# Kernel tuning notes

Measured on AMD Instinct MI355X. Metric: run time of the kernel, lower is better.

## Reference

```python
import jax, jax.numpy as jnp
import numpy as np

N_USER, N_MOVIE, N_EDGE = 200_000, 100_000, 4_000_000
D = 64  # feature dim = hidden_channels


def setup_inputs() -> dict:
    key = jax.random.key(0)
    ks = jax.random.split(key, 18)

    def W(k):
        return (jax.random.normal(k, (D, D), jnp.float32) / np.sqrt(D)).astype(jnp.float32)

    inp = {
        "x_user": jax.random.normal(ks[0], (N_USER, D), jnp.float32),
        "x_movie": jax.random.normal(ks[1], (N_MOVIE, D), jnp.float32),
        # layer 1, relation user->movie and movie->user
        "Wl1_um": W(ks[2]), "Wr1_um": W(ks[3]), "b1_um": jnp.zeros((D,), jnp.float32),
        "Wl1_mu": W(ks[4]), "Wr1_mu": W(ks[5]), "b1_mu": jnp.zeros((D,), jnp.float32),
        # layer 2
        "Wl2_um": W(ks[6]), "Wr2_um": W(ks[7]), "b2_um": jnp.zeros((D,), jnp.float32),
        "Wl2_mu": W(ks[8]), "Wr2_mu": W(ks[9]), "b2_mu": jnp.zeros((D,), jnp.float32),
        # rating edges: user_idx[e] rates movie_idx[e]; reverse relation reuses them swapped
        "user_idx": jax.random.randint(ks[10], (N_EDGE,), 0, N_USER, jnp.int64 if jax.config.jax_enable_x64 else jnp.int32),
        "movie_idx": jax.random.randint(ks[11], (N_EDGE,), 0, N_MOVIE, jnp.int64 if jax.config.jax_enable_x64 else jnp.int32),
    }
    return inp


def _sage(x_src, x_dst, src_idx, dst_idx, Wl, bl, Wr, n_dst):
    # PyG SAGEConv: lin_l(mean_aggr(x_j)) + bias + lin_r(x_dst)
    msg = x_src[src_idx]                                   # [E, D] gather
    s = jax.ops.segment_sum(msg, dst_idx, num_segments=n_dst)
    cnt = jax.ops.segment_sum(jnp.ones((msg.shape[0], 1), msg.dtype), dst_idx,
                              num_segments=n_dst)
    mean = s / jnp.maximum(cnt, 1.0)                       # degree-0 rows -> 0
    return mean @ Wl + bl + x_dst @ Wr


def reference(x_user, x_movie,
              Wl1_um, Wr1_um, b1_um, Wl1_mu, Wr1_mu, b1_mu,
              Wl2_um, Wr2_um, b2_um, Wl2_mu, Wr2_mu, b2_mu,
              user_idx, movie_idx):
    # layer 1 (per-relation SAGEConv, relu)
    m1 = jax.nn.relu(_sage(x_user, x_movie, user_idx, movie_idx,
                           Wl1_um, b1_um, Wr1_um, N_MOVIE))
    u1 = jax.nn.relu(_sage(x_movie, x_user, movie_idx, user_idx,
                           Wl1_mu, b1_mu, Wr1_mu, N_USER))
    # layer 2 (no activation)
    m2 = _sage(u1, m1, user_idx, movie_idx, Wl2_um, b2_um, Wr2_um, N_MOVIE)
    u2 = _sage(m1, u1, movie_idx, user_idx, Wl2_mu, b2_mu, Wr2_mu, N_USER)
    # concat the x_dict outputs (user then movie) into one array
    return jnp.concatenate([u2, m2], axis=0)
```

## Files before the change

### kernel.cpp

```cpp
#include <hip/hip_runtime.h>

#define NU 200000
#define NM 100000
#define NE 4000000
#define D  64

#define BDST 128
#define BU_BKTS ((NU + BDST - 1) / BDST)
#define BM_BKTS ((NM + BDST - 1) / BDST)
#define NBKT (BU_BKTS + BM_BKTS)
#define NBLK 256
#define CHUNK ((NE + NBLK - 1) / NBLK)

typedef unsigned int uint_t;
typedef unsigned short ushort_t;
typedef __attribute__((ext_vector_type(8))) short short8_t;
typedef __attribute__((ext_vector_type(4))) float f32x4_t;

__device__ __forceinline__ ushort_t f2bf(float f) {
  uint_t u = __float_as_uint(f);
  return (ushort_t)((u + 0x7FFFu + ((u >> 16) & 1u)) >> 16);
}
__device__ __forceinline__ float bflo(uint_t p) { return __uint_as_float(p << 16); }
__device__ __forceinline__ float bfhi(uint_t p) { return __uint_as_float(p & 0xFFFF0000u); }

__global__ __launch_bounds__(256) void cast_k(const float* __restrict__ xu,
                                              const float* __restrict__ xm,
                                              ushort_t* __restrict__ xu_h,
                                              ushort_t* __restrict__ xm_h) {
  const int n_u = NU * D / 4, n_m = NM * D / 4;
  const int stride = gridDim.x * blockDim.x;
  for (int i = blockIdx.x * blockDim.x + threadIdx.x; i < n_u + n_m; i += stride) {
    const bool isu = (i < n_u);
    const float4 v = isu ? ((const float4*)xu)[i] : ((const float4*)xm)[i - n_u];
    ushort4 o;
    o.x = f2bf(v.x); o.y = f2bf(v.y); o.z = f2bf(v.z); o.w = f2bf(v.w);
    if (isu) ((ushort4*)xu_h)[i] = o;
    else     ((ushort4*)xm_h)[i - n_u] = o;
  }
}

__global__ __launch_bounds__(256) void wprep_k(
    const float* __restrict__ W0, const float* __restrict__ W1,
    const float* __restrict__ W2, const float* __restrict__ W3,
    const float* __restrict__ W4, const float* __restrict__ W5,
    const float* __restrict__ W6, const float* __restrict__ W7,
    ushort_t* __restrict__ frag) {
  const int idx = blockIdx.x * 256 + threadIdx.x;
  if (idx >= 8 * 512) return;
  const int lane = idx & 63;
  const int h = (idx >> 6) & 1;
  const int t = (idx >> 7) & 3;
  const int mat = idx >> 9;
  const float* W = mat == 0 ? W0 : mat == 1 ? W1 : mat == 2 ? W2 : mat == 3 ? W3
                 : mat == 4 ? W4 : mat == 5 ? W5 : mat == 6 ? W6 : W7;
  const int col = t * 16 + (lane & 15);
  const int kb = h * 32 + (lane >> 4) * 8;
#pragma unroll
  for (int j = 0; j < 8; ++j)
    frag[(size_t)idx * 8 + j] = f2bf(W[(kb + j) * D + col]);
}

__global__ __launch_bounds__(256) void hist_k(const int* __restrict__ uidx,
                                              const int* __restrict__ midx,
                                              int* __restrict__ C_u,
                                              int* __restrict__ C_m) {
  __shared__ int h[NBKT];
  for (int i = threadIdx.x; i < NBKT; i += 256) h[i] = 0;
  __syncthreads();
  const int base = blockIdx.x * CHUNK;
  const int lim = min(base + CHUNK, NE);
  for (int e = base + threadIdx.x; e < lim; e += 256) {
    atomicAdd(&h[uidx[e] >> 7], 1);
    atomicAdd(&h[BU_BKTS + (midx[e] >> 7)], 1);
  }
  __syncthreads();
  for (int i = threadIdx.x; i < BU_BKTS; i += 256) C_u[(size_t)blockIdx.x * BU_BKTS + i] = h[i];
  for (int i = threadIdx.x; i < BM_BKTS; i += 256) C_m[(size_t)blockIdx.x * BM_BKTS + i] = h[BU_BKTS + i];
}

__global__ __launch_bounds__(256) void colscan_k(int* __restrict__ C_u,
                                                 int* __restrict__ C_m,
                                                 int* __restrict__ tot_u,
                                                 int* __restrict__ tot_m) {
  const int t = blockIdx.x * blockDim.x + threadIdx.x;
  if (t < BU_BKTS) {
    int run = 0;
    for (int blk = 0; blk < NBLK; ++blk) {
      const size_t idx = (size_t)blk * BU_BKTS + t;
      const int v = C_u[idx];
      C_u[idx] = run;
      run += v;
    }
    tot_u[t] = run;
  } else if (t < NBKT) {
    const int b = t - BU_BKTS;
    int run = 0;
    for (int blk = 0; blk < NBLK; ++blk) {
      const size_t idx = (size_t)blk * BM_BKTS + b;
      const int v = C_m[idx];
      C_m[idx] = run;
      run += v;
    }
    tot_m[b] = run;
  }
}

__device__ void scan_inline(const int* __restrict__ in, int* __restrict__ out,
                            int n, int* partial) {
  const int tid = threadIdx.x;
  const int chunk = (n + 1023) / 1024;
  const int s = tid * chunk;
  const int e = min(s + chunk, n);
  int sum = 0;
  for (int i = s; i < e; ++i) sum += in[i];
  partial[tid] = sum;
  __syncthreads();
  for (int off = 1; off < 1024; off <<= 1) {
    int v = (tid >= off) ? partial[tid - off] : 0;
    __syncthreads();
    if (tid >= off) partial[tid] += v;
    __syncthreads();
  }
  int run = (tid == 0) ? 0 : partial[tid - 1];
  for (int i = s; i < e; ++i) {
    out[i] = run;
    run += in[i];
  }
  if (tid == 1023) out[n] = partial[1023];
}

__global__ __launch_bounds__(1024) void bucketscan_k(const int* __restrict__ tot_u,
                                                     int* __restrict__ bb_u,
                                                     const int* __restrict__ tot_m,
                                                     int* __restrict__ bb_m) {
  __shared__ int partial[1024];
  scan_inline(tot_u, bb_u, BU_BKTS, partial);
  __syncthreads();
  scan_inline(tot_m, bb_m, BM_BKTS, partial);
}

__global__ __launch_bounds__(256) void part_k(const int* __restrict__ uidx,
                                              const int* __restrict__ midx,
                                              const int* __restrict__ C_u,
                                              const int* __restrict__ C_m,
                                              const int* __restrict__ bb_u,
                                              const int* __restrict__ bb_m,
                                              int* __restrict__ rec_u,
                                              int* __restrict__ rec_m) {
  __shared__ int cur[NBKT];
  for (int i = threadIdx.x; i < BU_BKTS; i += 256)
    cur[i] = bb_u[i] + C_u[(size_t)blockIdx.x * BU_BKTS + i];
  for (int i = threadIdx.x; i < BM_BKTS; i += 256)
    cur[BU_BKTS + i] = bb_m[i] + C_m[(size_t)blockIdx.x * BM_BKTS + i];
  __syncthreads();
  const int base = blockIdx.x * CHUNK;
  const int lim = min(base + CHUNK, NE);
  for (int e = base + threadIdx.x; e < lim; e += 256) {
    const int u = uidx[e];
    const int m = midx[e];
    const int pu = atomicAdd(&cur[u >> 7], 1);
    rec_u[pu] = (m << 7) | (u & (BDST - 1));
    const int pm = atomicAdd(&cur[BU_BKTS + (m >> 7)], 1);
    rec_m[pm] = (u << 7) | (m & (BDST - 1));
  }
}

__global__ __launch_bounds__(256) void sort_k(const int* __restrict__ rec_m,
                                              const int* __restrict__ rec_u,
                                              const int* __restrict__ bb_m,
                                              const int* __restrict__ bb_u,
                                              int* __restrict__ adj_m,
                                              int* __restrict__ adj_u,
                                              int* __restrict__ rowp_m,
                                              int* __restrict__ rowp_u) {
  __shared__ int cnt[BDST];
  __shared__ int off[BDST];
  __shared__ int tmp[BDST];
  const bool is_m = (blockIdx.x < BM_BKTS);
  const int bkt = is_m ? blockIdx.x : blockIdx.x - BM_BKTS;
  const int* recs = is_m ? rec_m : rec_u;
  const int* bb   = is_m ? bb_m : bb_u;
  int* adj  = is_m ? adj_m : adj_u;
  int* rowp = is_m ? rowp_m : rowp_u;
  const int nDst = is_m ? NM : NU;
  const int tid = threadIdx.x;

  for (int i = tid; i < BDST; i += 256) cnt[i] = 0;
  __syncthreads();
  const int rbeg = bb[bkt], rend = bb[bkt + 1];
  for (int j = rbeg + tid; j < rend; j += 256)
    atomicAdd(&cnt[recs[j] & (BDST - 1)], 1);
  __syncthreads();

  if (tid < BDST) tmp[tid] = cnt[tid];
  __syncthreads();
  for (int o = 1; o < BDST; o <<= 1) {
    int v = 0;
    if (tid < BDST && tid >= o) v = tmp[tid - o];
    __syncthreads();
    if (tid < BDST && tid >= o) tmp[tid] += v;
    __syncthreads();
  }
  if (tid < BDST) off[tid] = (tid == 0) ? 0 : tmp[tid - 1];
  __syncthreads();

  if (tid < BDST) {
    const int node = bkt * BDST + tid;
    if (node < nDst) rowp[node] = rbeg + off[tid];
  }
  if (blockIdx.x == 0 && tid == 0) rowp_m[NM] = NE;
  if (blockIdx.x == BM_BKTS && tid == 0) rowp_u[NU] = NE;

  if (tid < BDST) cnt[tid] = 0;
  __syncthreads();
  for (int j = rbeg + tid; j < rend; j += 256) {
    const int q = recs[j];
    const int dl = q & (BDST - 1);
    const int pos = atomicAdd(&cnt[dl], 1);
    adj[rbeg + off[dl] + pos] = q >> 7;
  }
}

__device__ __forceinline__ void agg_node16(const uint2* __restrict__ x2,
                                           const int* __restrict__ rowp,
                                           const int* __restrict__ adj,
                                           uint2* __restrict__ mean_h2,
                                           int node, int g, int q) {
  const int beg = rowp[node];
  const int end = rowp[node + 1];
  float a0 = 0.f, a1 = 0.f, a2 = 0.f, a3 = 0.f;
  int j = beg;
  for (; j + 16 <= end; j += 16) {
    const int e0 = adj[j + g];
    const int e1 = adj[j + 4 + g];
    const int e2 = adj[j + 8 + g];
    const int e3 = adj[j + 12 + g];
    const uint2 p0 = x2[(size_t)e0 * 16 + q];
    const uint2 p1 = x2[(size_t)e1 * 16 + q];
    const uint2 p2 = x2[(size_t)e2 * 16 + q];
    const uint2 p3 = x2[(size_t)e3 * 16 + q];
    a0 += (bflo(p0.x) + bflo(p1.x)) + (bflo(p2.x) + bflo(p3.x));
    a1 += (bfhi(p0.x) + bfhi(p1.x)) + (bfhi(p2.x) + bfhi(p3.x));
    a2 += (bflo(p0.y) + bflo(p1.y)) + (bflo(p2.y) + bflo(p3.y));
    a3 += (bfhi(p0.y) + bfhi(p1.y)) + (bfhi(p2.y) + bfhi(p3.y));
  }
  for (; j + 4 <= end; j += 4) {
    const int e = adj[j + g];
    const uint2 p = x2[(size_t)e * 16 + q];
    a0 += bflo(p.x); a1 += bfhi(p.x); a2 += bflo(p.y); a3 += bfhi(p.y);
  }
  if (j < end && g < end - j) {
    const int e = adj[j + g];
    const uint2 p = x2[(size_t)e * 16 + q];
    a0 += bflo(p.x); a1 += bfhi(p.x); a2 += bflo(p.y); a3 += bfhi(p.y);
  }
  a0 += __shfl_xor(a0, 16); a1 += __shfl_xor(a1, 16);
  a2 += __shfl_xor(a2, 16); a3 += __shfl_xor(a3, 16);
  a0 += __shfl_xor(a0, 32); a1 += __shfl_xor(a1, 32);
  a2 += __shfl_xor(a2, 32); a3 += __shfl_xor(a3, 32);
  if (g == 0) {
    const float inv = 1.0f / fmaxf((float)(end - beg), 1.0f);
    uint2 o;
    o.x = (uint_t)f2bf(a0 * inv) | ((uint_t)f2bf(a1 * inv) << 16);
    o.y = (uint_t)f2bf(a2 * inv) | ((uint_t)f2bf(a3 * inv) << 16);
    mean_h2[(size_t)node * 16 + q] = o;
  }
}

__global__ __launch_bounds__(256) void csr_both_h(const uint2* __restrict__ xu2,
                                                  const uint2* __restrict__ xm2,
                                                  const int* __restrict__ rowp_u,
                                                  const int* __restrict__ rowp_m,
                                                  const int* __restrict__ adj_u,
                                                  const int* __restrict__ adj_m,
                                                  uint2* __restrict__ mean_u2,
                                                  uint2* __restrict__ mean_m2) {
  const int lane = threadIdx.x & 63;
  const int g = lane >> 4;
  const int q = lane & 15;
  const int wid  = (blockIdx.x * blockDim.x + threadIdx.x) >> 6;
  const int W    = (gridDim.x * blockDim.x) >> 6;
  const int WM   = W / 3;
  if (wid < WM) {
    for (int node = wid; node < NM; node += WM)
      agg_node16(xu2, rowp_m, adj_m, mean_m2, node, g, q);
  } else {
    const int uw = wid - WM, UW = W - WM;
    for (int node = uw; node < NU; node += UW)
      agg_node16(xm2, rowp_u, adj_u, mean_u2, node, g, q);
  }
}

__global__ __launch_bounds__(256) void node_mfma_k(
    const ushort_t* __restrict__ mean_u, const ushort_t* __restrict__ mean_m,
    const ushort_t* __restrict__ xu_h,   const ushort_t* __restrict__ xm_h,
    const ushort_t* __restrict__ fragL_um, const ushort_t* __restrict__ fragR_um,
    const ushort_t* __restrict__ fragL_mu, const ushort_t* __restrict__ fragR_mu,
    const float* __restrict__ b_um, const float* __restrict__ b_mu,
    float* __restrict__ outf_u, float* __restrict__ outf_m,
    ushort_t* __restrict__ outh_u, ushort_t* __restrict__ outh_m, int mode) {
  const int lane = threadIdx.x & 63;
  const int wid  = (blockIdx.x * blockDim.x + threadIdx.x) >> 6;
  const int W    = (gridDim.x * blockDim.x) >> 6;
  const int WM   = W / 3;

  const ushort_t *mean, *xh, *fL, *fR;
  const float* bias;
  float* outf;
  ushort_t* outh;
  int nt, t0, tstride;
  if (wid < WM) {
    mean = mean_m; xh = xm_h; fL = fragL_um; fR = fragR_um; bias = b_um;
    outf = outf_m; outh = outh_m; nt = NM / 16; t0 = wid; tstride = WM;
  } else {
    mean = mean_u; xh = xu_h; fL = fragL_mu; fR = fragR_mu; bias = b_mu;
    outf = outf_u; outh = outh_u; nt = NU / 16; t0 = wid - WM; tstride = W - WM;
  }

  short8_t bl[4][2], br[4][2];
#pragma unroll
  for (int t = 0; t < 4; ++t)
#pragma unroll
    for (int h = 0; h < 2; ++h) {
      bl[t][h] = *(const short8_t*)&fL[(size_t)((t * 2 + h) * 64 + lane) * 8];
      br[t][h] = *(const short8_t*)&fR[(size_t)((t * 2 + h) * 64 + lane) * 8];
    }
  const int colb = lane & 15;
  const int kq = lane >> 4;
  float bv[4];
#pragma unroll
  for (int t = 0; t < 4; ++t) bv[t] = bias[t * 16 + colb];

  for (int tile = t0; tile < nt; tile += tstride) {
    const int base = tile * 16;
    const ushort_t* mrow = mean + (size_t)(base + colb) * D + kq * 8;
    const ushort_t* xrow = xh   + (size_t)(base + colb) * D + kq * 8;
    const short8_t am0 = *(const short8_t*)(mrow);
    const short8_t am1 = *(const short8_t*)(mrow + 32);
    const short8_t ax0 = *(const short8_t*)(xrow);
    const short8_t ax1 = *(const short8_t*)(xrow + 32);
#pragma unroll
    for (int t = 0; t < 4; ++t) {
      f32x4_t acc = {bv[t], bv[t], bv[t], bv[t]};
      acc = __builtin_amdgcn_mfma_f32_16x16x32_bf16(am0, bl[t][0], acc, 0, 0, 0);
      acc = __builtin_amdgcn_mfma_f32_16x16x32_bf16(am1, bl[t][1], acc, 0, 0, 0);
      acc = __builtin_amdgcn_mfma_f32_16x16x32_bf16(ax0, br[t][0], acc, 0, 0, 0);
      acc = __builtin_amdgcn_mfma_f32_16x16x32_bf16(ax1, br[t][1], acc, 0, 0, 0);
      const int col = t * 16 + colb;
#pragma unroll
      for (int j = 0; j < 4; ++j) {
        const int node = base + kq * 4 + j;
        if (mode) {
          outh[(size_t)node * D + col] = f2bf(fmaxf(acc[j], 0.f));
        } else {
          outf[(size_t)node * D + col] = acc[j];
        }
      }
    }
  }
}

extern "C" void kernel_launch(void* const* d_in, const int* in_sizes, int n_in,
                              void* d_out, int out_size, void* d_ws, size_t ws_size,
                              hipStream_t stream) {
  const float* x_user  = (const float*)d_in[0];
  const float* x_movie = (const float*)d_in[1];
  const float* Wl1_um = (const float*)d_in[2];
  const float* Wr1_um = (const float*)d_in[3];
  const float* b1_um  = (const float*)d_in[4];
  const float* Wl1_mu = (const float*)d_in[5];
  const float* Wr1_mu = (const float*)d_in[6];
  const float* b1_mu  = (const float*)d_in[7];
  const float* Wl2_um = (const float*)d_in[8];
  const float* Wr2_um = (const float*)d_in[9];
  const float* b2_um  = (const float*)d_in[10];
  const float* Wl2_mu = (const float*)d_in[11];
  const float* Wr2_mu = (const float*)d_in[12];
  const float* b2_mu  = (const float*)d_in[13];
  const int* uidx = (const int*)d_in[14];
  const int* midx = (const int*)d_in[15];

  char* ws = (char*)d_ws;
  ushort_t* mean_u = (ushort_t*)ws; ws += (size_t)NU * D * sizeof(ushort_t);
  ushort_t* mean_m = (ushort_t*)ws; ws += (size_t)NM * D * sizeof(ushort_t);
  ushort_t* xu_h = (ushort_t*)ws;   ws += (size_t)NU * D * sizeof(ushort_t);
  ushort_t* xm_h = (ushort_t*)ws;   ws += (size_t)NM * D * sizeof(ushort_t);
  ushort_t* u1_h = (ushort_t*)ws;   ws += (size_t)NU * D * sizeof(ushort_t);
  ushort_t* m1_h = (ushort_t*)ws;   ws += (size_t)NM * D * sizeof(ushort_t);
  int* adj_u  = (int*)ws;           ws += (size_t)NE * sizeof(int);
  int* adj_m  = (int*)ws;           ws += (size_t)NE * sizeof(int);
  int* rowp_u = (int*)ws;           ws += ((size_t)NU + 1) * sizeof(int);
  int* rowp_m = (int*)ws;           ws += ((size_t)NM + 1) * sizeof(int);
  int* tot_u  = (int*)ws;           ws += (size_t)BU_BKTS * sizeof(int);
  int* tot_m  = (int*)ws;           ws += (size_t)BM_BKTS * sizeof(int);
  int* bb_u   = (int*)ws;           ws += ((size_t)BU_BKTS + 1) * sizeof(int);
  int* bb_m   = (int*)ws;           ws += ((size_t)BM_BKTS + 1) * sizeof(int);
  ushort_t* fragW = (ushort_t*)ws;  ws += (size_t)8 * 512 * 8 * sizeof(ushort_t);

  int* rec_u = (int*)u1_h;
  int* rec_m = rec_u + NE;
  int* C_u   = (int*)mean_u;
  int* C_m   = C_u + (size_t)NBLK * BU_BKTS;

  float* u2 = (float*)d_out;
  float* m2 = (float*)d_out + (size_t)NU * D;

  const dim3 blk(256);

  cast_k<<<2048, blk, 0, stream>>>(x_user, x_movie, xu_h, xm_h);
  wprep_k<<<16, blk, 0, stream>>>(Wl1_um, Wr1_um, Wl1_mu, Wr1_mu,
                                  Wl2_um, Wr2_um, Wl2_mu, Wr2_mu, fragW);
  hist_k<<<NBLK, blk, 0, stream>>>(uidx, midx, C_u, C_m);
  colscan_k<<<(NBKT + 255) / 256, blk, 0, stream>>>(C_u, C_m, tot_u, tot_m);
  bucketscan_k<<<1, 1024, 0, stream>>>(tot_u, bb_u, tot_m, bb_m);
  part_k<<<NBLK, blk, 0, stream>>>(uidx, midx, C_u, C_m, bb_u, bb_m, rec_u, rec_m);
  sort_k<<<NBKT, blk, 0, stream>>>(rec_m, rec_u, bb_m, bb_u,
                                   adj_m, adj_u, rowp_m, rowp_u);

  csr_both_h<<<3072, blk, 0, stream>>>((const uint2*)xu_h, (const uint2*)xm_h,
                                       rowp_u, rowp_m, adj_u, adj_m,
                                       (uint2*)mean_u, (uint2*)mean_m);
  node_mfma_k<<<1024, blk, 0, stream>>>(mean_u, mean_m, xu_h, xm_h,
                                        fragW + 0 * 4096, fragW + 1 * 4096,
                                        fragW + 2 * 4096, fragW + 3 * 4096,
                                        b1_um, b1_mu,
                                        nullptr, nullptr, u1_h, m1_h, 1);

  csr_both_h<<<3072, blk, 0, stream>>>((const uint2*)u1_h, (const uint2*)m1_h,
                                       rowp_u, rowp_m, adj_u, adj_m,
                                       (uint2*)mean_u, (uint2*)mean_m);
  node_mfma_k<<<1024, blk, 0, stream>>>(mean_u, mean_m, u1_h, m1_h,
                                        fragW + 4 * 4096, fragW + 5 * 4096,
                                        fragW + 6 * 4096, fragW + 7 * 4096,
                                        b2_um, b2_mu,
                                        u2, m2, nullptr, nullptr, 0);
}
```

Baseline: 610.1 us.

## Quantize layer-1 activations to uint8 for layer-2 neighbor aggregation

Layer-1 ReLU outputs are quantized to 8-bit unsigned values, using a per-node-type global max tracked by atomics in the MFMA kernel. Layer-2 mean aggregation then gathers these bytes and accumulates them as packed 16-bit integer lanes. This halves the gather traffic of the bandwidth-bound layer-2 aggregation. The cost is an extra quantization pass, an atomic max reduction, and precision loss from 8-bit activations, which could break accuracy tolerance.

New measurement: 681.0 us. 11.6% more time.

```diff
diff --git a/kernel.cpp b/kernel.cpp
--- a/kernel.cpp
+++ b/kernel.cpp
@@ -14,6 +14,7 @@
 
 typedef unsigned int uint_t;
 typedef unsigned short ushort_t;
+typedef unsigned char uchar_t;
 typedef __attribute__((ext_vector_type(8))) short short8_t;
 typedef __attribute__((ext_vector_type(4))) float f32x4_t;
 
@@ -292,6 +293,128 @@
   }
 }
 
+__device__ __forceinline__ void agg_node8q(const uint2* __restrict__ xq,
+                                           const int* __restrict__ rowp,
+                                           const int* __restrict__ adj,
+                                           uint4* __restrict__ mean_h4,
+                                           float s, int node, int g, int q) {
+  const int beg = rowp[node];
+  const int end = rowp[node + 1];
+  uint_t accA = 0, accB = 0, accC = 0, accD = 0;
+  int j = beg;
+  for (; j + 16 <= end; j += 16) {
+    const int e0 = adj[j + g];
+    const int e1 = adj[j + 8 + g];
+    const uint2 p0 = xq[(size_t)e0 * 8 + q];
+    const uint2 p1 = xq[(size_t)e1 * 8 + q];
+    accA += (p0.x & 0x00FF00FFu) + (p1.x & 0x00FF00FFu);
+    accB += ((p0.x >> 8) & 0x00FF00FFu) + ((p1.x >> 8) & 0x00FF00FFu);
+    accC += (p0.y & 0x00FF00FFu) + (p1.y & 0x00FF00FFu);
+    accD += ((p0.y >> 8) & 0x00FF00FFu) + ((p1.y >> 8) & 0x00FF00FFu);
+  }
+  for (; j + 8 <= end; j += 8) {
+    const int e = adj[j + g];
+    const uint2 p = xq[(size_t)e * 8 + q];
+    accA += p.x & 0x00FF00FFu;
+    accB += (p.x >> 8) & 0x00FF00FFu;
+    accC += p.y & 0x00FF00FFu;
+    accD += (p.y >> 8) & 0x00FF00FFu;
+  }
+  if (j < end && g < end - j) {
+    const int e = adj[j + g];
+    const uint2 p = xq[(size_t)e * 8 + q];
+    accA += p.x & 0x00FF00FFu;
+    accB += (p.x >> 8) & 0x00FF00FFu;
+    accC += p.y & 0x00FF00FFu;
+    accD += (p.y >> 8) & 0x00FF00FFu;
+  }
+  accA += (uint_t)__shfl_xor((int)accA, 8);
+  accB += (uint_t)__shfl_xor((int)accB, 8);
+  accC += (uint_t)__shfl_xor((int)accC, 8);
+  accD += (uint_t)__shfl_xor((int)accD, 8);
+  accA += (uint_t)__shfl_xor((int)accA, 16);
+  accB += (uint_t)__shfl_xor((int)accB, 16);
+  accC += (uint_t)__shfl_xor((int)accC, 16);
+  accD += (uint_t)__shfl_xor((int)accD, 16);
+  accA += (uint_t)__shfl_xor((int)accA, 32);
+  accB += (uint_t)__shfl_xor((int)accB, 32);
+  accC += (uint_t)__shfl_xor((int)accC, 32);
+  accD += (uint_t)__shfl_xor((int)accD, 32);
+  if (g == 0) {
+    const float inv = s / fmaxf((float)(end - beg), 1.0f);
+    const float f0 = (float)(accA & 0xFFFFu) * inv;
+    const float f1 = (float)(accB & 0xFFFFu) * inv;
+    const float f2 = (float)(accA >> 16) * inv;
+    const float f3 = (float)(accB >> 16) * inv;
+    const float f4 = (float)(accC & 0xFFFFu) * inv;
+    const float f5 = (float)(accD & 0xFFFFu) * inv;
+    const float f6 = (float)(accC >> 16) * inv;
+    const float f7 = (float)(accD >> 16) * inv;
+    uint4 o;
+    o.x = (uint_t)f2bf(f0) | ((uint_t)f2bf(f1) << 16);
+    o.y = (uint_t)f2bf(f2) | ((uint_t)f2bf(f3) << 16);
+    o.z = (uint_t)f2bf(f4) | ((uint_t)f2bf(f5) << 16);
+    o.w = (uint_t)f2bf(f6) | ((uint_t)f2bf(f7) << 16);
+    mean_h4[(size_t)node * 8 + q] = o;
+  }
+}
+
+__global__ __launch_bounds__(256) void csr_both_q(const uint2* __restrict__ uq2,
+                                                  const uint2* __restrict__ mq2,
+                                                  const int* __restrict__ rowp_u,
+                                                  const int* __restrict__ rowp_m,
+                                                  const int* __restrict__ adj_u,
+                                                  const int* __restrict__ adj_m,
+                                                  uint4* __restrict__ mean_u4,
+                                                  uint4* __restrict__ mean_m4,
+                                                  const uint_t* __restrict__ gmax) {
+  const float s_u = __uint_as_float(gmax[0]) * (1.0f / 255.0f);
+  const float s_m = __uint_as_float(gmax[1]) * (1.0f / 255.0f);
+  const int lane = threadIdx.x & 63;
+  const int g = lane >> 3;
+  const int q = lane & 7;
+  const int wid  = (blockIdx.x * blockDim.x + threadIdx.x) >> 6;
+  const int W    = (gridDim.x * blockDim.x) >> 6;
+  const int WM   = W / 3;
+  if (wid < WM) {
+    for (int node = wid; node < NM; node += WM)
+      agg_node8q(uq2, rowp_m, adj_m, mean_m4, s_u, node, g, q);
+  } else {
+    const int uw = wid - WM, UW = W - WM;
+    for (int node = uw; node < NU; node += UW)
+      agg_node8q(mq2, rowp_u, adj_u, mean_u4, s_m, node, g, q);
+  }
+}
+
+__global__ __launch_bounds__(256) void quant_k(const uint4* __restrict__ u1h4,
+                                               const uint4* __restrict__ m1h4,
+                                               const uint_t* __restrict__ gmax,
+                                               uint2* __restrict__ u1q2,
+                                               uint2* __restrict__ m1q2) {
+  const float qs_u = 255.0f / fmaxf(__uint_as_float(gmax[0]), 1e-20f);
+  const float qs_m = 255.0f / fmaxf(__uint_as_float(gmax[1]), 1e-20f);
+  const int n_u = NU * D / 8, n_m = NM * D / 8;
+  const int stride = gridDim.x * blockDim.x;
+  for (int i = blockIdx.x * blockDim.x + threadIdx.x; i < n_u + n_m; i += stride) {
+    const bool isu = (i < n_u);
+    const uint4 v = isu ? u1h4[i] : m1h4[i - n_u];
+    const float qs = isu ? qs_u : qs_m;
+    uint_t b0 = (uint_t)fminf(rintf(bflo(v.x) * qs), 255.f);
+    uint_t b1 = (uint_t)fminf(rintf(bfhi(v.x) * qs), 255.f);
+    uint_t b2 = (uint_t)fminf(rintf(bflo(v.y) * qs), 255.f);
+    uint_t b3 = (uint_t)fminf(rintf(bfhi(v.y) * qs), 255.f);
+    uint_t b4 = (uint_t)fminf(rintf(bflo(v.z) * qs), 255.f);
+    uint_t b5 = (uint_t)fminf(rintf(bfhi(v.z) * qs), 255.f);
+    uint_t b6 = (uint_t)fminf(rintf(bflo(v.w) * qs), 255.f);
+    uint_t b7 = (uint_t)fminf(rintf(bfhi(v.w) * qs), 255.f);
+    uint2 o;
+    o.x = b0 | (b1 << 8) | (b2 << 16) | (b3 << 24);
+    o.y = b4 | (b5 << 8) | (b6 << 16) | (b7 << 24);
+    if (isu) u1q2[i] = o;
+    else     m1q2[i - n_u] = o;
+  }
+}
+
 __global__ __launch_bounds__(256) void node_mfma_k(
     const ushort_t* __restrict__ mean_u, const ushort_t* __restrict__ mean_m,
     const ushort_t* __restrict__ xu_h,   const ushort_t* __restrict__ xm_h,
@@ -299,7 +422,8 @@
     const ushort_t* __restrict__ fragL_mu, const ushort_t* __restrict__ fragR_mu,
     const float* __restrict__ b_um, const float* __restrict__ b_mu,
     float* __restrict__ outf_u, float* __restrict__ outf_m,
-    ushort_t* __restrict__ outh_u, ushort_t* __restrict__ outh_m, int mode) {
+    ushort_t* __restrict__ outh_u, ushort_t* __restrict__ outh_m,
+    uint_t* __restrict__ gmax, int mode) {
   const int lane = threadIdx.x & 63;
   const int wid  = (blockIdx.x * blockDim.x + threadIdx.x) >> 6;
   const int W    = (gridDim.x * blockDim.x) >> 6;
@@ -309,13 +433,13 @@
   const float* bias;
   float* outf;
   ushort_t* outh;
-  int nt, t0, tstride;
+  int nt, t0, tstride, gidx;
   if (wid < WM) {
     mean = mean_m; xh = xm_h; fL = fragL_um; fR = fragR_um; bias = b_um;
-    outf = outf_m; outh = outh_m; nt = NM / 16; t0 = wid; tstride = WM;
+    outf = outf_m; outh = outh_m; nt = NM / 16; t0 = wid; tstride = WM; gidx = 1;
   } else {
     mean = mean_u; xh = xu_h; fL = fragL_mu; fR = fragR_mu; bias = b_mu;
-    outf = outf_u; outh = outh_u; nt = NU / 16; t0 = wid - WM; tstride = W - WM;
+    outf = outf_u; outh = outh_u; nt = NU / 16; t0 = wid - WM; tstride = W - WM; gidx = 0;
   }
 
   short8_t bl[4][2], br[4][2];
@@ -332,6 +456,7 @@
 #pragma unroll
   for (int t = 0; t < 4; ++t) bv[t] = bias[t * 16 + colb];
 
+  float lmax = 0.f;
   for (int tile = t0; tile < nt; tile += tstride) {
     const int base = tile * 16;
     const ushort_t* mrow = mean + (size_t)(base + colb) * D + kq * 8;
@@ -352,12 +477,23 @@
       for (int j = 0; j < 4; ++j) {
         const int node = base + kq * 4 + j;
         if (mode) {
-          outh[(size_t)node * D + col] = f2bf(fmaxf(acc[j], 0.f));
+          const float r = fmaxf(acc[j], 0.f);
+          lmax = fmaxf(lmax, r);
+          outh[(size_t)node * D + col] = f2bf(r);
         } else {
           outf[(size_t)node * D + col] = acc[j];
         }
       }
     }
+  }
+  if (mode) {
+    lmax = fmaxf(lmax, __shfl_xor(lmax, 1));
+    lmax = fmaxf(lmax, __shfl_xor(lmax, 2));
+    lmax = fmaxf(lmax, __shfl_xor(lmax, 4));
+    lmax = fmaxf(lmax, __shfl_xor(lmax, 8));
+    lmax = fmaxf(lmax, __shfl_xor(lmax, 16));
+    lmax = fmaxf(lmax, __shfl_xor(lmax, 32));
+    if (lane == 0) atomicMax(&gmax[gidx], __float_as_uint(lmax));
   }
 }
 
@@ -397,6 +533,9 @@
   int* bb_u   = (int*)ws;           ws += ((size_t)BU_BKTS + 1) * sizeof(int);
   int* bb_m   = (int*)ws;           ws += ((size_t)BM_BKTS + 1) * sizeof(int);
   ushort_t* fragW = (ushort_t*)ws;  ws += (size_t)8 * 512 * 8 * sizeof(ushort_t);
+  uchar_t* u1_q = (uchar_t*)ws;     ws += (size_t)NU * D;
+  uchar_t* m1_q = (uchar_t*)ws;     ws += (size_t)NM * D;
+  uint_t* gmax = (uint_t*)ws;       ws += 2 * sizeof(uint_t);
 
   int* rec_u = (int*)u1_h;
   int* rec_m = rec_u + NE;
@@ -408,6 +547,7 @@
 
   const dim3 blk(256);
 
+  hipMemsetAsync(gmax, 0, 2 * sizeof(uint_t), stream);
   cast_k<<<2048, blk, 0, stream>>>(x_user, x_movie, xu_h, xm_h);
   wprep_k<<<16, blk, 0, stream>>>(Wl1_um, Wr1_um, Wl1_mu, Wr1_mu,
                                   Wl2_um, Wr2_um, Wl2_mu, Wr2_mu, fragW);
@@ -425,14 +565,17 @@
                                         fragW + 0 * 4096, fragW + 1 * 4096,
                                         fragW + 2 * 4096, fragW + 3 * 4096,
                                         b1_um, b1_mu,
-                                        nullptr, nullptr, u1_h, m1_h, 1);
-
-  csr_both_h<<<3072, blk, 0, stream>>>((const uint2*)u1_h, (const uint2*)m1_h,
+                                        nullptr, nullptr, u1_h, m1_h, gmax, 1);
+
+  quant_k<<<2048, blk, 0, stream>>>((const uint4*)u1_h, (const uint4*)m1_h,
+                                    gmax, (uint2*)u1_q, (uint2*)m1_q);
+
+  csr_both_q<<<3072, blk, 0, stream>>>((const uint2*)u1_q, (const uint2*)m1_q,
                                        rowp_u, rowp_m, adj_u, adj_m,
-                                       (uint2*)mean_u, (uint2*)mean_m);
+                                       (uint4*)mean_u, (uint4*)mean_m, gmax);
   node_mfma_k<<<1024, blk, 0, stream>>>(mean_u, mean_m, u1_h, m1_h,
                                         fragW + 4 * 4096, fragW + 5 * 4096,
                                         fragW + 6 * 4096, fragW + 7 * 4096,
                                         b2_um, b2_mu,
-                                        u2, m2, nullptr, nullptr, 0);
-}
+                                        u2, m2, nullptr, nullptr, gmax, 0);
+}
```
